# Kernel optimization log

Hardware: AMD Instinct MI355X
Metric: run time of the kernel (lower is better)

The kernel has to match this reference:

```python
import jax, jax.numpy as jnp
import numpy as np

S, U, N, T, D = 512, 1024, 100000, 3, 20
N_NEG = 10
LAMBDA_REG = 0.01


def setup_inputs() -> dict:
    key = jax.random.key(0)
    ks = jax.random.split(key, 18)
    inp = {
        "x": jax.random.randint(ks[0], (S, U), 0, N),
        "x_time_segments": jax.random.randint(ks[1], (S, U), 0, T),
        "y": jax.random.randint(ks[2], (S, U), 0, N),
        "y_time_segments": jax.random.randint(ks[3], (S, U), 0, T),
        "neg_idx": jax.random.randint(ks[4], (S, U, N_NEG), 0, N),
        # vecs_use stacked: [time_segments, num_centroids, 20] (buffer, not a parameter)
        "vecs": jax.random.normal(ks[5], (T, N, D), dtype=jnp.float32) * 0.1,
        # parameters
        "time_emb": jax.random.normal(ks[6], (T, D), dtype=jnp.float32),
        "W1": jax.random.normal(ks[7], (3 * D, D), dtype=jnp.float32) * 0.1,
        "b1": jax.random.normal(ks[8], (D,), dtype=jnp.float32) * 0.01,
        "W2": jax.random.normal(ks[9], (D, 10), dtype=jnp.float32) * 0.1,
        "b2": jax.random.normal(ks[10], (10,), dtype=jnp.float32) * 0.01,
        "Wv1": jax.random.normal(ks[11], (D, D), dtype=jnp.float32) * 0.1,
        "bv1": jax.random.normal(ks[12], (D,), dtype=jnp.float32) * 0.01,
        "Wv2": jax.random.normal(ks[13], (D, 10), dtype=jnp.float32) * 0.1,
        "bv2": jax.random.normal(ks[14], (10,), dtype=jnp.float32) * 0.01,
        "Wadj": jax.random.normal(ks[15], (D, 10), dtype=jnp.float32) * 0.1,
        "badj": jax.random.normal(ks[16], (10,), dtype=jnp.float32) * 0.01,
    }
    return inp


def reference(x, x_time_segments, y, y_time_segments, neg_idx,
              vecs, time_emb, W1, b1, W2, b2, Wv1, bv1, Wv2, bv2, Wadj, badj):
    xseg, yseg = x_time_segments, y_time_segments
    # per-element embedding gather (replaces the per-segment masked scatter loop)
    x_emb = vecs[xseg, x]                 # [S, U, 20]
    y_emb = vecs[yseg, y]                 # [S, U, 20]

    # time-aware embedding MLP: cat(e_i, t_i, t_j) -> relu -> linear (fused over all S*U)
    xi_in = jnp.concatenate([x_emb, time_emb[xseg], time_emb[yseg]], axis=-1)  # [S, U, 60]
    xi = jax.nn.relu(xi_in @ W1 + b1) @ W2 + b2                                # [S, U, 10]

    # vec embedding MLP applied to all centroid tables (vec_0/1/2_output stacked)
    vec_out = jax.nn.relu(vecs @ Wv1 + bv1) @ Wv2 + bv2                        # [T, N, 10]
    # positive sample = same MLP on y_emb
    pos = jax.nn.relu(y_emb @ Wv1 + bv1) @ Wv2 + bv2                           # [S, U, 10]

    # negative samples: 10 random rows from the current segment's vec_out
    neg = vec_out[xseg[..., None], neg_idx]                                    # [S, U, 10, 10]

    pos_d = jnp.linalg.norm(xi - pos, axis=-1)                                 # [S, U]
    neg_d = jnp.linalg.norm(xi[..., None, :] - neg, axis=-1)                   # [S, U, 10]

    loss = -jnp.sum(jax.nn.log_sigmoid(neg_d - pos_d[..., None])) / (S * U)

    # L2 regularization over nn.Parameters (vecs_use tables are buffers, excluded)
    params = (time_emb, W1, b1, W2, b2, Wv1, bv1, Wv2, bv2, Wadj, badj)
    reg = sum(jnp.linalg.norm(p) for p in params)
    return loss + LAMBDA_REG * reg
```

## Files before the change

### kernel.cpp

```cpp
#include <hip/hip_runtime.h>
#include <math.h>

constexpr int Ncent = 100000, NNEG = 10;
constexpr int SU = 524288;
constexpr int TN = 300000;
constexpr float LAMBDA = 0.01f;
constexpr int PRE_BLOCKS = 1172;
constexpr int LOSS_BLOCKS = SU / 512;

constexpr float AENC = 127.0f / 0.30f, ADEC = 0.30f / 127.0f;
constexpr float VENC = 127.0f / 0.20f, VDEC = 0.20f / 127.0f;

constexpr int A1B = 32;
constexpr int VOBY = 16;

__device__ __forceinline__ float log_sigmoid_f(float z) {
    return fminf(z, 0.f) - __logf(1.f + __expf(-fabsf(z)));
}
__device__ __forceinline__ unsigned pk4b(float a, float b, float c, float d, float enc) {
    int qa = min(255, max(0, __float2int_rn(fmaf(a, enc, 128.f))));
    int qb = min(255, max(0, __float2int_rn(fmaf(b, enc, 128.f))));
    int qc = min(255, max(0, __float2int_rn(fmaf(c, enc, 128.f))));
    int qd = min(255, max(0, __float2int_rn(fmaf(d, enc, 128.f))));
    return (unsigned)qa | ((unsigned)qb << 8) | ((unsigned)qc << 16) | ((unsigned)qd << 24);
}
__device__ __forceinline__ float ub2f(unsigned w, int b) {
    return (float)((w >> (8 * b)) & 0xffu);
}

__global__ __launch_bounds__(256) void precomp_kernel(
    const float* __restrict__ vecs, const float* __restrict__ time_emb,
    const float* __restrict__ W1, const float* __restrict__ b1,
    const float* __restrict__ Wv1, const float* __restrict__ bv1,
    const float* __restrict__ Wv2, const float* __restrict__ bv2,
    const float* __restrict__ W2, const float* __restrict__ b2,
    const float* __restrict__ Wadj, const float* __restrict__ badj,
    unsigned char* __restrict__ A1q, unsigned char* __restrict__ VOq,
    float* __restrict__ TT, float* __restrict__ reg_out)
{
    __shared__ __align__(16) float sW1a[400];
    __shared__ __align__(16) float sWv1[400];
    __shared__ __align__(16) float sWv2[200];
    __shared__ float sbv1[20], sbv2[10];
    const int t = threadIdx.x;
    for (int i = t; i < 400; i += 256) { sW1a[i] = W1[i]; sWv1[i] = Wv1[i]; }
    for (int i = t; i < 200; i += 256) sWv2[i] = Wv2[i];
    if (t < 20) sbv1[t] = bv1[t];
    if (t < 10) sbv2[t] = bv2[t];
    __syncthreads();

    if (blockIdx.x == 0 && t < 180) {
        const int a = t / 60, b = (t / 20) % 3, j = t % 20;
        float s = b1[j];
        #pragma unroll
        for (int k = 0; k < 20; ++k) {
            s = fmaf(time_emb[a * 20 + k], W1[(20 + k) * 20 + j], s);
            s = fmaf(time_emb[b * 20 + k], W1[(40 + k) * 20 + j], s);
        }
        TT[t] = s - 128.f * ADEC;
    }

    const int row = blockIdx.x * 256 + t;
    if (row < TN) {
        float v[20];
        {
            const float4* p = (const float4*)(vecs + (size_t)row * 20);
            #pragma unroll
            for (int i = 0; i < 5; ++i) { float4 q = p[i]; v[4*i]=q.x; v[4*i+1]=q.y; v[4*i+2]=q.z; v[4*i+3]=q.w; }
        }
        {
            float a[20];
            #pragma unroll
            for (int j = 0; j < 20; ++j) a[j] = 0.f;
            #pragma unroll
            for (int k = 0; k < 20; ++k) {
                const float vk = v[k];
                #pragma unroll
                for (int q = 0; q < 5; ++q) {
                    const float4 w = ((const float4*)sW1a)[k * 5 + q];
                    a[4*q]   = fmaf(vk, w.x, a[4*q]);
                    a[4*q+1] = fmaf(vk, w.y, a[4*q+1]);
                    a[4*q+2] = fmaf(vk, w.z, a[4*q+2]);
                    a[4*q+3] = fmaf(vk, w.w, a[4*q+3]);
                }
            }
            unsigned w[5];
            #pragma unroll
            for (int i = 0; i < 5; ++i) w[i] = pk4b(a[4*i], a[4*i+1], a[4*i+2], a[4*i+3], AENC);
            unsigned* q = (unsigned*)(A1q + (size_t)row * A1B);
            *(uint4*)q = make_uint4(w[0], w[1], w[2], w[3]);
            q[4] = w[4];
        }
        {
            float h[20];
            #pragma unroll
            for (int j = 0; j < 20; ++j) h[j] = sbv1[j];
            #pragma unroll
            for (int k = 0; k < 20; ++k) {
                const float vk = v[k];
                #pragma unroll
                for (int q = 0; q < 5; ++q) {
                    const float4 w = ((const float4*)sWv1)[k * 5 + q];
                    h[4*q]   = fmaf(vk, w.x, h[4*q]);
                    h[4*q+1] = fmaf(vk, w.y, h[4*q+1]);
                    h[4*q+2] = fmaf(vk, w.z, h[4*q+2]);
                    h[4*q+3] = fmaf(vk, w.w, h[4*q+3]);
                }
            }
            #pragma unroll
            for (int j = 0; j < 20; ++j) h[j] = fmaxf(h[j], 0.f);
            float o[10];
            #pragma unroll
            for (int j = 0; j < 10; ++j) o[j] = sbv2[j];
            #pragma unroll
            for (int k = 0; k < 20; ++k) {
                const float hk = h[k];
                #pragma unroll
                for (int q = 0; q < 5; ++q) {
                    const float2 w = ((const float2*)sWv2)[k * 5 + q];
                    o[2*q]   = fmaf(hk, w.x, o[2*q]);
                    o[2*q+1] = fmaf(hk, w.y, o[2*q+1]);
                }
            }
            unsigned* p = (unsigned*)(VOq + (size_t)row * VOBY);
            *(uint4*)p = make_uint4(pk4b(o[0], o[1], o[2], o[3], VENC),
                                    pk4b(o[4], o[5], o[6], o[7], VENC),
                                    pk4b(o[8], o[9], 0.f, 0.f, VENC),
                                    0u);
        }
    }

    if (blockIdx.x == 1) {
        __shared__ float wsum[4];
        const float* ps[11] = {time_emb, W1, b1, W2, b2, Wv1, bv1, Wv2, bv2, Wadj, badj};
        const int    ns[11] = {60, 1200, 20, 200, 10, 400, 20, 200, 10, 200, 10};
        float reg = 0.f;
        #pragma unroll
        for (int p = 0; p < 11; ++p) {
            float r = 0.f;
            const float* q = ps[p];
            for (int i = t; i < ns[p]; i += 256) { float v = q[i]; r = fmaf(v, v, r); }
            #pragma unroll
            for (int off = 32; off > 0; off >>= 1) r += __shfl_down(r, off);
            if ((t & 63) == 0) wsum[t >> 6] = r;
            __syncthreads();
            reg += sqrtf(wsum[0] + wsum[1] + wsum[2] + wsum[3]);
            __syncthreads();
        }
        if (t == 0) reg_out[0] = reg;
    }
}

struct G { uint4 a; unsigned a4; uint4 p; uint4 n[10]; };

__device__ __forceinline__ float elem_loss(const G& g, int xs, int ys,
                                           const float* __restrict__ sTT,
                                           const float* __restrict__ W2,
                                           const float* __restrict__ b2)
{
    float h1[20];
    {
        const unsigned wa[5] = {g.a.x, g.a.y, g.a.z, g.a.w, g.a4};
        const int tb = xs * 60 + ys * 20;
        #pragma unroll
        for (int i = 0; i < 5; ++i) {
            #pragma unroll
            for (int b = 0; b < 4; ++b) {
                const int j = 4 * i + b;
                h1[j] = fmaxf(fmaf(ub2f(wa[i], b), ADEC, sTT[tb + j]), 0.f);
            }
        }
    }
    float xj[10];
    #pragma unroll
    for (int j = 0; j < 10; ++j) xj[j] = b2[j] + 128.f * VDEC;
    #pragma unroll
    for (int k = 0; k < 20; ++k) {
        const float hk = h1[k];
        #pragma unroll
        for (int j = 0; j < 10; ++j) xj[j] = fmaf(hk, W2[k * 10 + j], xj[j]);
    }
    float pos_d;
    {
        const unsigned pw[3] = {g.p.x, g.p.y, g.p.z};
        float d2 = 0.f;
        #pragma unroll
        for (int j = 0; j < 10; ++j) {
            float df = fmaf(-VDEC, ub2f(pw[j >> 2], j & 3), xj[j]);
            d2 = fmaf(df, df, d2);
        }
        pos_d = sqrtf(d2);
    }
    float lsum = 0.f;
    #pragma unroll
    for (int n = 0; n < 10; ++n) {
        const unsigned nw[3] = {g.n[n].x, g.n[n].y, g.n[n].z};
        float d2 = 0.f;
        #pragma unroll
        for (int j = 0; j < 10; ++j) {
            float df = fmaf(-VDEC, ub2f(nw[j >> 2], j & 3), xj[j]);
            d2 = fmaf(df, df, d2);
        }
        lsum += log_sigmoid_f(sqrtf(d2) - pos_d);
    }
    return lsum;
}

__global__ __launch_bounds__(256, 2) void loss_kernel(
    const int* __restrict__ x, const int* __restrict__ xsegp,
    const int* __restrict__ y, const int* __restrict__ ysegp,
    const int* __restrict__ nidx,
    const float* __restrict__ W2, const float* __restrict__ b2,
    const unsigned char* __restrict__ A1q, const unsigned char* __restrict__ VOq,
    const float* __restrict__ TT,
    double* __restrict__ acc)
{
    __shared__ float sTT[180];
    __shared__ float warp_part[4];
    const int t = threadIdx.x;
    if (t < 45) ((float4*)sTT)[t] = ((const float4*)TT)[t];
    __syncthreads();

    const int i0 = blockIdx.x * 256 + t;
    const int i1 = i0 + (SU >> 1);

    const int xv0 = x[i0], xs0 = xsegp[i0], yv0 = y[i0], ys0 = ysegp[i0];
    const int xv1 = x[i1], xs1 = xsegp[i1], yv1 = y[i1], ys1 = ysegp[i1];
    int nn0[10], nn1[10];
    {
        const int2* p0 = (const int2*)(nidx + (size_t)i0 * NNEG);
        const int2* p1 = (const int2*)(nidx + (size_t)i1 * NNEG);
        #pragma unroll
        for (int i = 0; i < 5; ++i) {
            int2 a = p0[i]; nn0[2*i] = a.x; nn0[2*i+1] = a.y;
            int2 b = p1[i]; nn1[2*i] = b.x; nn1[2*i+1] = b.y;
        }
    }

    G g0, g1;
    {
        const unsigned* pa = (const unsigned*)(A1q + (size_t)(xs0 * Ncent + xv0) * A1B);
        g0.a = *(const uint4*)pa; g0.a4 = pa[4];
        g0.p = *(const uint4*)(VOq + (size_t)(ys0 * Ncent + yv0) * VOBY);
        const unsigned char* vs = VOq + (size_t)xs0 * Ncent * VOBY;
        #pragma unroll
        for (int n = 0; n < 10; ++n) g0.n[n] = *(const uint4*)(vs + (size_t)nn0[n] * VOBY);
    }
    {
        const unsigned* pa = (const unsigned*)(A1q + (size_t)(xs1 * Ncent + xv1) * A1B);
        g1.a = *(const uint4*)pa; g1.a4 = pa[4];
        g1.p = *(const uint4*)(VOq + (size_t)(ys1 * Ncent + yv1) * VOBY);
        const unsigned char* vs = VOq + (size_t)xs1 * Ncent * VOBY;
        #pragma unroll
        for (int n = 0; n < 10; ++n) g1.n[n] = *(const uint4*)(vs + (size_t)nn1[n] * VOBY);
    }

    asm volatile("" :: "v"(g0.a.x), "v"(g0.a.y), "v"(g0.a.z), "v"(g0.a.w), "v"(g0.a4),
                       "v"(g0.p.x), "v"(g0.p.y), "v"(g0.p.z));
    #pragma unroll
    for (int n = 0; n < 10; ++n)
        asm volatile("" :: "v"(g0.n[n].x), "v"(g0.n[n].y), "v"(g0.n[n].z));
    float lsum = elem_loss(g0, xs0, ys0, sTT, W2, b2);

    asm volatile("" :: "v"(g1.a.x), "v"(g1.a.y), "v"(g1.a.z), "v"(g1.a.w), "v"(g1.a4),
                       "v"(g1.p.x), "v"(g1.p.y), "v"(g1.p.z));
    #pragma unroll
    for (int n = 0; n < 10; ++n)
        asm volatile("" :: "v"(g1.n[n].x), "v"(g1.n[n].y), "v"(g1.n[n].z));
    lsum += elem_loss(g1, xs1, ys1, sTT, W2, b2);

    #pragma unroll
    for (int off = 32; off > 0; off >>= 1) lsum += __shfl_down(lsum, off);
    if ((t & 63) == 0) warp_part[t >> 6] = lsum;
    __syncthreads();
    if (t == 0)
        atomicAdd(acc, (double)(warp_part[0] + warp_part[1] + warp_part[2] + warp_part[3]));
}

__global__ void finalize_kernel(const double* __restrict__ acc,
                                const float* __restrict__ reg_in,
                                float* __restrict__ out)
{
    out[0] = (float)(-acc[0] / (double)SU) + LAMBDA * reg_in[0];
}

extern "C" void kernel_launch(void* const* d_in, const int* in_sizes, int n_in,
                              void* d_out, int out_size, void* d_ws, size_t ws_size,
                              hipStream_t stream)
{
    const int*   x        = (const int*)d_in[0];
    const int*   xseg     = (const int*)d_in[1];
    const int*   y        = (const int*)d_in[2];
    const int*   yseg     = (const int*)d_in[3];
    const int*   nidx     = (const int*)d_in[4];
    const float* vecs     = (const float*)d_in[5];
    const float* time_emb = (const float*)d_in[6];
    const float* W1       = (const float*)d_in[7];
    const float* b1       = (const float*)d_in[8];
    const float* W2       = (const float*)d_in[9];
    const float* b2       = (const float*)d_in[10];
    const float* Wv1      = (const float*)d_in[11];
    const float* bv1      = (const float*)d_in[12];
    const float* Wv2      = (const float*)d_in[13];
    const float* bv2      = (const float*)d_in[14];
    const float* Wadj     = (const float*)d_in[15];
    const float* badj     = (const float*)d_in[16];

    char* ws = (char*)d_ws;
    unsigned char* A1q = (unsigned char*)(ws);
    unsigned char* VOq = (unsigned char*)(ws + 9601024);
    float*  TT  = (float*)(ws + 14401536);
    double* acc = (double*)(ws + 14402304);
    float*  reg = (float*)(ws + 14402368);

    hipMemsetAsync(acc, 0, 8, stream);
    precomp_kernel<<<PRE_BLOCKS, 256, 0, stream>>>(
        vecs, time_emb, W1, b1, Wv1, bv1, Wv2, bv2, W2, b2, Wadj, badj,
        A1q, VOq, TT, reg);
    loss_kernel<<<LOSS_BLOCKS, 256, 0, stream>>>(
        x, xseg, y, yseg, nidx, W2, b2, A1q, VOq, TT, acc);
    finalize_kernel<<<1, 1, 0, stream>>>(acc, reg, (float*)d_out);
}
```

Baseline: 178.2 us.

## Process one element per thread with inline-asm gather loads and explicit waitcnt

The loss kernel drops the two-elements-per-thread scheme and launches twice as many blocks, each thread handling a single element. The gathers are issued through inline-asm global_load_dwordx4 with a single s_waitcnt and a scheduling barrier, so all twelve loads are in flight before any compute starts. The negative-index loads become wider int4 loads, and the occupancy hint in launch_bounds is removed. The cost is less memory-level parallelism per thread, which now relies on more waves being resident, plus hand-written asm that the compiler cannot schedule around.

```diff
diff --git a/kernel.cpp b/kernel.cpp
--- a/kernel.cpp
+++ b/kernel.cpp
@@ -6,13 +6,16 @@
 constexpr int TN = 300000;
 constexpr float LAMBDA = 0.01f;
 constexpr int PRE_BLOCKS = 1172;
-constexpr int LOSS_BLOCKS = SU / 512;
+constexpr int LOSS_BLOCKS = SU / 256;
 
 constexpr float AENC = 127.0f / 0.30f, ADEC = 0.30f / 127.0f;
 constexpr float VENC = 127.0f / 0.20f, VDEC = 0.20f / 127.0f;
 
 constexpr int A1B = 32;
 constexpr int VOBY = 16;
+
+typedef unsigned int uint;
+typedef uint v4u __attribute__((ext_vector_type(4)));
 
 __device__ __forceinline__ float log_sigmoid_f(float z) {
     return fminf(z, 0.f) - __logf(1.f + __expf(-fabsf(z)));
@@ -26,6 +29,16 @@
 }
 __device__ __forceinline__ float ub2f(unsigned w, int b) {
     return (float)((w >> (8 * b)) & 0xffu);
+}
+__device__ __forceinline__ v4u gld4(const void* p) {
+    v4u d;
+    asm volatile("global_load_dwordx4 %0, %1, off" : "=v"(d) : "v"(p));
+    return d;
+}
+__device__ __forceinline__ uint gld1(const void* p) {
+    uint d;
+    asm volatile("global_load_dword %0, %1, off" : "=v"(d) : "v"(p));
+    return d;
 }
 
 __global__ __launch_bounds__(256) void precomp_kernel(
@@ -151,62 +164,7 @@
     }
 }
 
-struct G { uint4 a; unsigned a4; uint4 p; uint4 n[10]; };
-
-__device__ __forceinline__ float elem_loss(const G& g, int xs, int ys,
-                                           const float* __restrict__ sTT,
-                                           const float* __restrict__ W2,
-                                           const float* __restrict__ b2)
-{
-    float h1[20];
-    {
-        const unsigned wa[5] = {g.a.x, g.a.y, g.a.z, g.a.w, g.a4};
-        const int tb = xs * 60 + ys * 20;
-        #pragma unroll
-        for (int i = 0; i < 5; ++i) {
-            #pragma unroll
-            for (int b = 0; b < 4; ++b) {
-                const int j = 4 * i + b;
-                h1[j] = fmaxf(fmaf(ub2f(wa[i], b), ADEC, sTT[tb + j]), 0.f);
-            }
-        }
-    }
-    float xj[10];
-    #pragma unroll
-    for (int j = 0; j < 10; ++j) xj[j] = b2[j] + 128.f * VDEC;
-    #pragma unroll
-    for (int k = 0; k < 20; ++k) {
-        const float hk = h1[k];
-        #pragma unroll
-        for (int j = 0; j < 10; ++j) xj[j] = fmaf(hk, W2[k * 10 + j], xj[j]);
-    }
-    float pos_d;
-    {
-        const unsigned pw[3] = {g.p.x, g.p.y, g.p.z};
-        float d2 = 0.f;
-        #pragma unroll
-        for (int j = 0; j < 10; ++j) {
-            float df = fmaf(-VDEC, ub2f(pw[j >> 2], j & 3), xj[j]);
-            d2 = fmaf(df, df, d2);
-        }
-        pos_d = sqrtf(d2);
-    }
-    float lsum = 0.f;
-    #pragma unroll
-    for (int n = 0; n < 10; ++n) {
-        const unsigned nw[3] = {g.n[n].x, g.n[n].y, g.n[n].z};
-        float d2 = 0.f;
-        #pragma unroll
-        for (int j = 0; j < 10; ++j) {
-            float df = fmaf(-VDEC, ub2f(nw[j >> 2], j & 3), xj[j]);
-            d2 = fmaf(df, df, d2);
-        }
-        lsum += log_sigmoid_f(sqrtf(d2) - pos_d);
-    }
-    return lsum;
-}
-
-__global__ __launch_bounds__(256, 2) void loss_kernel(
+__global__ __launch_bounds__(256) void loss_kernel(
     const int* __restrict__ x, const int* __restrict__ xsegp,
     const int* __restrict__ y, const int* __restrict__ ysegp,
     const int* __restrict__ nidx,
@@ -221,54 +179,76 @@
     if (t < 45) ((float4*)sTT)[t] = ((const float4*)TT)[t];
     __syncthreads();
 
-    const int i0 = blockIdx.x * 256 + t;
-    const int i1 = i0 + (SU >> 1);
-
-    const int xv0 = x[i0], xs0 = xsegp[i0], yv0 = y[i0], ys0 = ysegp[i0];
-    const int xv1 = x[i1], xs1 = xsegp[i1], yv1 = y[i1], ys1 = ysegp[i1];
-    int nn0[10], nn1[10];
+    const int idx = blockIdx.x * 256 + t;
+    const int xv = x[idx], xs = xsegp[idx], yv = y[idx], ys = ysegp[idx];
+    int nn[10];
     {
-        const int2* p0 = (const int2*)(nidx + (size_t)i0 * NNEG);
-        const int2* p1 = (const int2*)(nidx + (size_t)i1 * NNEG);
+        const int* p = nidx + (size_t)idx * NNEG;
+        int4 a = *(const int4*)(p);
+        int4 b = *(const int4*)(p + 4);
+        int2 c = *(const int2*)(p + 8);
+        nn[0]=a.x; nn[1]=a.y; nn[2]=a.z; nn[3]=a.w;
+        nn[4]=b.x; nn[5]=b.y; nn[6]=b.z; nn[7]=b.w;
+        nn[8]=c.x; nn[9]=c.y;
+    }
+
+    const unsigned char* pa = A1q + (size_t)(xs * Ncent + xv) * A1B;
+    v4u  ga  = gld4(pa);
+    uint ga4 = gld1(pa + 16);
+    v4u  gp  = gld4(VOq + (size_t)(ys * Ncent + yv) * VOBY);
+    const unsigned char* vs = VOq + (size_t)xs * Ncent * VOBY;
+    v4u gn[10];
+    #pragma unroll
+    for (int n = 0; n < 10; ++n) gn[n] = gld4(vs + (size_t)nn[n] * VOBY);
+
+    asm volatile("s_waitcnt vmcnt(0)");
+    __builtin_amdgcn_sched_barrier(0);
+
+    float h1[20];
+    {
+        const unsigned wa[5] = {ga.x, ga.y, ga.z, ga.w, ga4};
+        const int tb = xs * 60 + ys * 20;
         #pragma unroll
         for (int i = 0; i < 5; ++i) {
-            int2 a = p0[i]; nn0[2*i] = a.x; nn0[2*i+1] = a.y;
-            int2 b = p1[i]; nn1[2*i] = b.x; nn1[2*i+1] = b.y;
-        }
-    }
-
-    G g0, g1;
+            #pragma unroll
+            for (int b = 0; b < 4; ++b) {
+                const int j = 4 * i + b;
+                h1[j] = fmaxf(fmaf(ub2f(wa[i], b), ADEC, sTT[tb + j]), 0.f);
+            }
+        }
+    }
+    float xj[10];
+    #pragma unroll
+    for (int j = 0; j < 10; ++j) xj[j] = b2[j] + 128.f * VDEC;
+    #pragma unroll
+    for (int k = 0; k < 20; ++k) {
+        const float hk = h1[k];
+        #pragma unroll
+        for (int j = 0; j < 10; ++j) xj[j] = fmaf(hk, W2[k * 10 + j], xj[j]);
+    }
+    float pos_d;
     {
-        const unsigned* pa = (const unsigned*)(A1q + (size_t)(xs0 * Ncent + xv0) * A1B);
-        g0.a = *(const uint4*)pa; g0.a4 = pa[4];
-        g0.p = *(const uint4*)(VOq + (size_t)(ys0 * Ncent + yv0) * VOBY);
-        const unsigned char* vs = VOq + (size_t)xs0 * Ncent * VOBY;
-        #pragma unroll
-        for (int n = 0; n < 10; ++n) g0.n[n] = *(const uint4*)(vs + (size_t)nn0[n] * VOBY);
-    }
-    {
-        const unsigned* pa = (const unsigned*)(A1q + (size_t)(xs1 * Ncent + xv1) * A1B);
-        g1.a = *(const uint4*)pa; g1.a4 = pa[4];
-        g1.p = *(const uint4*)(VOq + (size_t)(ys1 * Ncent + yv1) * VOBY);
-        const unsigned char* vs = VOq + (size_t)xs1 * Ncent * VOBY;
-        #pragma unroll
-        for (int n = 0; n < 10; ++n) g1.n[n] = *(const uint4*)(vs + (size_t)nn1[n] * VOBY);
-    }
-
-    asm volatile("" :: "v"(g0.a.x), "v"(g0.a.y), "v"(g0.a.z), "v"(g0.a.w), "v"(g0.a4),
-                       "v"(g0.p.x), "v"(g0.p.y), "v"(g0.p.z));
-    #pragma unroll
-    for (int n = 0; n < 10; ++n)
-        asm volatile("" :: "v"(g0.n[n].x), "v"(g0.n[n].y), "v"(g0.n[n].z));
-    float lsum = elem_loss(g0, xs0, ys0, sTT, W2, b2);
-
-    asm volatile("" :: "v"(g1.a.x), "v"(g1.a.y), "v"(g1.a.z), "v"(g1.a.w), "v"(g1.a4),
-                       "v"(g1.p.x), "v"(g1.p.y), "v"(g1.p.z));
-    #pragma unroll
-    for (int n = 0; n < 10; ++n)
-        asm volatile("" :: "v"(g1.n[n].x), "v"(g1.n[n].y), "v"(g1.n[n].z));
-    lsum += elem_loss(g1, xs1, ys1, sTT, W2, b2);
-
+        float d2 = 0.f;
+        const unsigned pw[3] = {gp.x, gp.y, gp.z};
+        #pragma unroll
+        for (int j = 0; j < 10; ++j) {
+            float df = fmaf(-VDEC, ub2f(pw[j >> 2], j & 3), xj[j]);
+            d2 = fmaf(df, df, d2);
+        }
+        pos_d = sqrtf(d2);
+    }
+    float lsum = 0.f;
+    #pragma unroll
+    for (int n = 0; n < 10; ++n) {
+        const unsigned nw[3] = {gn[n].x, gn[n].y, gn[n].z};
+        float d2 = 0.f;
+        #pragma unroll
+        for (int j = 0; j < 10; ++j) {
+            float df = fmaf(-VDEC, ub2f(nw[j >> 2], j & 3), xj[j]);
+            d2 = fmaf(df, df, d2);
+        }
+        lsum += log_sigmoid_f(sqrtf(d2) - pos_d);
+    }
     #pragma unroll
     for (int off = 32; off > 0; off >>= 1) lsum += __shfl_down(lsum, off);
     if ((t & 63) == 0) warp_part[t >> 6] = lsum;
```

Result: slower. 197.4 us (+10.8%).
